# Performance work log

Hardware: AMD Instinct MI355X
Metric: run time of the kernel (lower is better)

Reference implementation:

```python
import jax, jax.numpy as jnp
import numpy as np

B, N = 2, 512
D_NODE, D_EDGE, D_HID, H = 128, 64, 128, 8
DH = D_HID // H  # per-head dim = 16
SCALE = 1.0 / (D_HID ** 0.5)  # note: scale uses full d_hid as in source


def setup_inputs() -> dict:
    key = jax.random.key(0)
    k1, k2, k3, k4 = jax.random.split(key, 4)
    node_features = jax.random.normal(k1, (B, N, D_NODE), dtype=jnp.float32)
    edge_features = jax.random.normal(k2, (B, N, N, D_EDGE), dtype=jnp.float32)
    mask = jnp.ones((B, N, N), dtype=bool)
    # Linear weights (stored as (in, out); math identical to torch x @ W.T)
    W_node = jax.random.normal(k3, (D_NODE, 3 * D_HID), dtype=jnp.float32) / np.sqrt(D_NODE)
    W_edge = jax.random.normal(k4, (D_EDGE, 3 * D_HID), dtype=jnp.float32) / np.sqrt(D_EDGE)
    return {"node_features": node_features, "edge_features": edge_features,
            "mask": mask, "W_node": W_node, "W_edge": W_edge}


def _split_heads_node(x):
    # (b, n, h*c) -> (b, h, n, c)
    b, n, hc = x.shape
    return x.reshape(b, n, H, hc // H).transpose(0, 2, 1, 3)


def _split_heads_edge(x):
    # (b, n, m, h*c) -> (b, h, n, m, c)
    b, n, m, hc = x.shape
    return x.reshape(b, n, m, H, hc // H).transpose(0, 3, 1, 2, 4)


def reference(node_features, edge_features, mask, W_node, W_edge):
    # node qkv: (b, n, 3*d_hid) -> (b, h, n, 3*dh) -> chunk
    qkv_n = _split_heads_node(node_features @ W_node)
    q_node, k_node, v_node = jnp.split(qkv_n, 3, axis=-1)  # each (b,h,n,dh)
    # edge qkv: (b, n, n, 3*d_hid) -> (b, h, n, n, 3*dh) -> chunk
    qkv_e = _split_heads_edge(edge_features @ W_edge)
    q_edge, k_edge, v_edge = jnp.split(qkv_e, 3, axis=-1)  # each (b,h,n,n,dh)

    q = q_node[:, :, :, None, :] + q_edge   # (b,h,i,j,dh)
    k = k_node[:, :, None, :, :] + k_edge   # (b,h,i,j,dh)
    v = v_node[:, :, None, :, :] + v_edge   # (b,h,i,j,dh)

    dots = SCALE * jnp.einsum('bhijd,bhijd->bhij', q, k)
    attn = jax.nn.softmax(dots, axis=-1)
    out = jnp.einsum('bhij,bhijd->bhid', attn, v)  # (b,h,n,dh)
    # (b,h,n,dh) -> (b,n,h*dh)
    b, h, n, dh = out.shape
    return out.transpose(0, 2, 1, 3).reshape(b, n, h * dh)
```

## Files before the change

kernel.cpp:

```cpp
#include <hip/hip_runtime.h>
#include <hip/hip_bf16.h>

#define NN 512
#define OC 384
#define S2F 0.12751694f

typedef __attribute__((ext_vector_type(8))) short short8;
typedef __attribute__((ext_vector_type(4))) float f32x4;

__device__ __forceinline__ unsigned short f2bf(float x) {
    unsigned u = __builtin_bit_cast(unsigned, x);
    u = (u + 0x7fffu + ((u >> 16) & 1u)) >> 16;
    return (unsigned short)u;
}

__device__ __forceinline__ ushort4 cvt4(f32x4 a) {
    union { ushort4 u4; __hip_bfloat162 h[2]; } r;
    r.h[0] = __float22bfloat162_rn(make_float2(a[0], a[1]));
    r.h[1] = __float22bfloat162_rn(make_float2(a[2], a[3]));
    return r.u4;
}

__global__ __launch_bounds__(256) void prep0_kernel(
    const float* __restrict__ Wn, const float* __restrict__ We,
    const float* __restrict__ node,
    unsigned short* __restrict__ WtN, unsigned short* __restrict__ WtE,
    unsigned short* __restrict__ nodeBf)
{
    int idx = blockIdx.x * 256 + threadIdx.x;
    if (idx < 24576) {
        int o = idx >> 6, k = idx & 63;
        WtE[idx] = f2bf(We[k * OC + o]);
    } else if (idx < 24576 + 49152) {
        int id = idx - 24576;
        int o = id >> 7, k = id & 127;
        WtN[id] = f2bf(Wn[k * OC + o]);
    } else {
        int id = idx - 73728;
        nodeBf[id] = f2bf(node[id]);
    }
}

__global__ __launch_bounds__(256) void prep1_kernel(
    const unsigned short* __restrict__ nodeBf,
    const unsigned short* __restrict__ WtN,
    float* __restrict__ qnF,
    float* __restrict__ nodeKV)
{
    const int t = threadIdx.x;
    const int w = t >> 6;
    const int lane = t & 63;
    const int lj = lane & 15;
    const int quad = lane >> 4;
    const int nbase = blockIdx.x * 32;

    short8 bfr[2][4];
#pragma unroll
    for (int nt = 0; nt < 2; ++nt)
#pragma unroll
        for (int ks = 0; ks < 4; ++ks)
            bfr[nt][ks] = *reinterpret_cast<const short8*>(
                nodeBf + (size_t)(nbase + nt * 16 + lj) * 128 + ks * 32 + quad * 8);

#pragma unroll
    for (int m = 0; m < 6; ++m) {
        int ot = (6 * w + m) * 16;
        short8 afr[4];
#pragma unroll
        for (int ks = 0; ks < 4; ++ks)
            afr[ks] = *reinterpret_cast<const short8*>(
                WtN + (size_t)(ot + lj) * 128 + ks * 32 + quad * 8);
#pragma unroll
        for (int nt = 0; nt < 2; ++nt) {
            f32x4 acc = {0.f, 0.f, 0.f, 0.f};
#pragma unroll
            for (int ks = 0; ks < 4; ++ks)
                acc = __builtin_amdgcn_mfma_f32_16x16x32_bf16(afr[ks], bfr[nt][ks], acc, 0, 0, 0);
            int n = nbase + nt * 16 + lj;
            int bb = n >> 9, ii = n & 511;
#pragma unroll
            for (int r = 0; r < 4; ++r) {
                int o = ot + quad * 4 + r;
                int h = o / 48, rem = o - h * 48;
                size_t base = (size_t)(bb * 8 + h) * NN + ii;
                if (rem < 16) {
                    qnF[base * 16 + rem] = acc[r];
                } else {
                    int d = (rem - 16) & 15;
                    int isv = (rem >= 32) ? 4 : 0;
                    nodeKV[base * 32 + (d >> 2) * 8 + isv + (d & 3)] = acc[r];
                }
            }
        }
    }
}

__global__ __launch_bounds__(512, 4) void rt_attn_main(
    const float* __restrict__ edge,
    const float* __restrict__ qnF,
    const float* __restrict__ nodeKV,
    const unsigned short* __restrict__ WtE,
    float* __restrict__ out)
{
    __shared__ unsigned short sE[2][64 * 72];
    const int bi = blockIdx.x;
    const int b = bi >> 9;
    const int i = bi & 511;
    const int t = threadIdx.x;
    const int h = t >> 6;
    const int lane = t & 63;
    const int lj = lane & 15;
    const int quad = lane >> 4;

    const int sj0 = t >> 4;
    const int sj1 = sj0 + 32;
    const int sc = (t & 15) * 4;

    const float* eBase = edge + (size_t)bi * NN * 64;
    f32x4 pf0, pf1;
    pf0 = *reinterpret_cast<const f32x4*>(eBase + (size_t)sj0 * 64 + sc);
    pf1 = *reinterpret_cast<const f32x4*>(eBase + (size_t)sj1 * 64 + sc);

    short8 afr[3][2];
#pragma unroll
    for (int T = 0; T < 3; ++T)
#pragma unroll
        for (int sec = 0; sec < 2; ++sec)
            afr[T][sec] = *reinterpret_cast<const short8*>(
                WtE + (size_t)(h * 48 + T * 16 + lj) * 64 + sec * 32 + quad * 8);

    const f32x4 qn = *reinterpret_cast<const f32x4*>(
        qnF + ((size_t)(b * 8 + h) * NN + i) * 16 + quad * 4);

    float l = 0.f;
    float oa[4] = {0.f, 0.f, 0.f, 0.f};
    const float* kvBase = nodeKV + (size_t)(b * 8 + h) * NN * 32;

    {
        *reinterpret_cast<ushort4*>(&sE[0][sj0 * 72 + sc]) = cvt4(pf0);
        *reinterpret_cast<ushort4*>(&sE[0][sj1 * 72 + sc]) = cvt4(pf1);
    }
    __syncthreads();

    for (int tt = 0; tt < 8; ++tt) {
        const int cur = tt & 1;
        f32x4 ka[4], va[4];
#pragma unroll
        for (int jn = 0; jn < 4; ++jn) {
            const float* kvp = kvBase + (size_t)(tt * 64 + jn * 16 + lj) * 32 + quad * 8;
            ka[jn] = *reinterpret_cast<const f32x4*>(kvp);
            va[jn] = *reinterpret_cast<const f32x4*>(kvp + 4);
        }
        if (tt < 7) {
            const float* nb = eBase + (size_t)(tt + 1) * 4096;
            pf0 = *reinterpret_cast<const f32x4*>(nb + (size_t)sj0 * 64 + sc);
            pf1 = *reinterpret_cast<const f32x4*>(nb + (size_t)sj1 * 64 + sc);
        }
        float dp[4];
        f32x4 fvv[4];
#pragma unroll
        for (int jn = 0; jn < 4; ++jn) {
            const int jrow = jn * 16 + lj;
            short8 b0 = *reinterpret_cast<const short8*>(&sE[cur][jrow * 72 + quad * 8]);
            short8 b1 = *reinterpret_cast<const short8*>(&sE[cur][jrow * 72 + 32 + quad * 8]);
            f32x4 fq = qn;
            fq = __builtin_amdgcn_mfma_f32_16x16x32_bf16(afr[0][0], b0, fq, 0, 0, 0);
            fq = __builtin_amdgcn_mfma_f32_16x16x32_bf16(afr[0][1], b1, fq, 0, 0, 0);
            f32x4 fk = ka[jn];
            fk = __builtin_amdgcn_mfma_f32_16x16x32_bf16(afr[1][0], b0, fk, 0, 0, 0);
            fk = __builtin_amdgcn_mfma_f32_16x16x32_bf16(afr[1][1], b1, fk, 0, 0, 0);
            f32x4 fv = va[jn];
            fv = __builtin_amdgcn_mfma_f32_16x16x32_bf16(afr[2][0], b0, fv, 0, 0, 0);
            fv = __builtin_amdgcn_mfma_f32_16x16x32_bf16(afr[2][1], b1, fv, 0, 0, 0);
            fvv[jn] = fv;
            float d0 = fq[0] * fk[0];
            d0 = fmaf(fq[1], fk[1], d0);
            d0 = fmaf(fq[2], fk[2], d0);
            d0 = fmaf(fq[3], fk[3], d0);
            dp[jn] = d0;
        }
        float t16[4], t32[4], wg[4];
#pragma unroll
        for (int jn = 0; jn < 4; ++jn) t16[jn] = __shfl_xor(dp[jn], 16);
#pragma unroll
        for (int jn = 0; jn < 4; ++jn) dp[jn] += t16[jn];
#pragma unroll
        for (int jn = 0; jn < 4; ++jn) t32[jn] = __shfl_xor(dp[jn], 32);
#pragma unroll
        for (int jn = 0; jn < 4; ++jn) {
            wg[jn] = exp2f((dp[jn] + t32[jn]) * S2F);
            l += wg[jn];
        }
#pragma unroll
        for (int jn = 0; jn < 4; ++jn)
#pragma unroll
            for (int r = 0; r < 4; ++r)
                oa[r] = fmaf(wg[jn], fvv[jn][r], oa[r]);
        if (tt < 7) {
            *reinterpret_cast<ushort4*>(&sE[cur ^ 1][sj0 * 72 + sc]) = cvt4(pf0);
            *reinterpret_cast<ushort4*>(&sE[cur ^ 1][sj1 * 72 + sc]) = cvt4(pf1);
            __syncthreads();
        }
    }

#pragma unroll
    for (int off = 1; off <= 8; off <<= 1) {
        l += __shfl_xor(l, off);
#pragma unroll
        for (int r = 0; r < 4; ++r) oa[r] += __shfl_xor(oa[r], off);
    }
    if (lj == 0) {
        float inv = 1.0f / l;
        f32x4 o4;
#pragma unroll
        for (int r = 0; r < 4; ++r) o4[r] = oa[r] * inv;
        *reinterpret_cast<f32x4*>(out + (size_t)bi * 128 + h * 16 + quad * 4) = o4;
    }
}

extern "C" void kernel_launch(void* const* d_in, const int* in_sizes, int n_in,
                              void* d_out, int out_size, void* d_ws, size_t ws_size,
                              hipStream_t stream) {
    const float* node = (const float*)d_in[0];
    const float* edge = (const float*)d_in[1];
    const float* Wn = (const float*)d_in[3];
    const float* We = (const float*)d_in[4];
    float* out = (float*)d_out;

    char* ws = (char*)d_ws;
    float* qnF = (float*)ws;
    float* nodeKV = (float*)(ws + 524288);
    unsigned short* WtE = (unsigned short*)(ws + 1572864);
    unsigned short* WtN = (unsigned short*)(ws + 1622016);
    unsigned short* nodeBf = (unsigned short*)(ws + 1720320);

    prep0_kernel<<<800, 256, 0, stream>>>(Wn, We, node, WtN, WtE, nodeBf);
    prep1_kernel<<<32, 256, 0, stream>>>(nodeBf, WtN, qnF, nodeKV);
    rt_attn_main<<<2 * NN, 512, 0, stream>>>(edge, qnF, nodeKV, WtE, out);
}
```

Before: 242.2 us.

## Load edge tiles straight into registers and split heads across blocks

The main attention kernel stops staging edge features through shared memory. Each lane now loads its own fp32 edge values directly into registers, converts them to bf16 MFMA operands, and software-pipelines the next group's loads behind the current MFMAs. Work is repartitioned so each block handles 4 heads for one row, with each wave covering 2 heads over half of the j range. A small shared-memory reduction merges the two halves. This removes the per-tile __syncthreads and LDS traffic, but each edge row is now read from global memory by two blocks, and register pressure rises.

```diff
diff --git a/kernel.cpp b/kernel.cpp
--- a/kernel.cpp
+++ b/kernel.cpp
@@ -7,6 +7,8 @@
 
 typedef __attribute__((ext_vector_type(8))) short short8;
 typedef __attribute__((ext_vector_type(4))) float f32x4;
+
+#define LD4(p) (*reinterpret_cast<const f32x4*>(p))
 
 __device__ __forceinline__ unsigned short f2bf(float x) {
     unsigned u = __builtin_bit_cast(unsigned, x);
@@ -14,11 +16,13 @@
     return (unsigned short)u;
 }
 
-__device__ __forceinline__ ushort4 cvt4(f32x4 a) {
-    union { ushort4 u4; __hip_bfloat162 h[2]; } r;
+__device__ __forceinline__ short8 cvt8(f32x4 a, f32x4 b) {
+    union { short8 s8; __hip_bfloat162 h[4]; } r;
     r.h[0] = __float22bfloat162_rn(make_float2(a[0], a[1]));
     r.h[1] = __float22bfloat162_rn(make_float2(a[2], a[3]));
-    return r.u4;
+    r.h[2] = __float22bfloat162_rn(make_float2(b[0], b[1]));
+    r.h[3] = __float22bfloat162_rn(make_float2(b[2], b[3]));
+    return r.s8;
 }
 
 __global__ __launch_bounds__(256) void prep0_kernel(
@@ -95,126 +99,149 @@
     }
 }
 
-__global__ __launch_bounds__(512, 4) void rt_attn_main(
+template <int REFILL>
+__device__ __forceinline__ void group_step(
+    f32x4& E0, f32x4& E1, f32x4& E2, f32x4& E3,
+    f32x4& K0, f32x4& V0, f32x4& K1, f32x4& V1,
+    const float* ep, const float* kq0, const float* kq1,
+    const short8 (&afr)[2][3][2],
+    const f32x4& qn0, const f32x4& qn1,
+    float& l0, float& l1, float (&oa0)[4], float (&oa1)[4])
+{
+    short8 b0 = cvt8(E0, E1);
+    short8 b1 = cvt8(E2, E3);
+    if constexpr (REFILL) {
+        E0 = LD4(ep); E1 = LD4(ep + 4); E2 = LD4(ep + 32); E3 = LD4(ep + 36);
+    }
+    f32x4 fq = __builtin_amdgcn_mfma_f32_16x16x32_bf16(afr[0][0][0], b0, qn0, 0, 0, 0);
+    fq = __builtin_amdgcn_mfma_f32_16x16x32_bf16(afr[0][0][1], b1, fq, 0, 0, 0);
+    f32x4 fk = __builtin_amdgcn_mfma_f32_16x16x32_bf16(afr[0][1][0], b0, K0, 0, 0, 0);
+    fk = __builtin_amdgcn_mfma_f32_16x16x32_bf16(afr[0][1][1], b1, fk, 0, 0, 0);
+    f32x4 fv = __builtin_amdgcn_mfma_f32_16x16x32_bf16(afr[0][2][0], b0, V0, 0, 0, 0);
+    fv = __builtin_amdgcn_mfma_f32_16x16x32_bf16(afr[0][2][1], b1, fv, 0, 0, 0);
+    if constexpr (REFILL) { K0 = LD4(kq0); V0 = LD4(kq0 + 4); }
+    float dp = fq[0] * fk[0];
+    dp = fmaf(fq[1], fk[1], dp);
+    dp = fmaf(fq[2], fk[2], dp);
+    dp = fmaf(fq[3], fk[3], dp);
+    dp += __shfl_xor(dp, 16);
+    dp += __shfl_xor(dp, 32);
+    float wg = exp2f(dp * S2F);
+    l0 += wg;
+#pragma unroll
+    for (int r = 0; r < 4; ++r) oa0[r] = fmaf(wg, fv[r], oa0[r]);
+    f32x4 gq = __builtin_amdgcn_mfma_f32_16x16x32_bf16(afr[1][0][0], b0, qn1, 0, 0, 0);
+    gq = __builtin_amdgcn_mfma_f32_16x16x32_bf16(afr[1][0][1], b1, gq, 0, 0, 0);
+    f32x4 gk = __builtin_amdgcn_mfma_f32_16x16x32_bf16(afr[1][1][0], b0, K1, 0, 0, 0);
+    gk = __builtin_amdgcn_mfma_f32_16x16x32_bf16(afr[1][1][1], b1, gk, 0, 0, 0);
+    f32x4 gv = __builtin_amdgcn_mfma_f32_16x16x32_bf16(afr[1][2][0], b0, V1, 0, 0, 0);
+    gv = __builtin_amdgcn_mfma_f32_16x16x32_bf16(afr[1][2][1], b1, gv, 0, 0, 0);
+    if constexpr (REFILL) { K1 = LD4(kq1); V1 = LD4(kq1 + 4); }
+    float dq = gq[0] * gk[0];
+    dq = fmaf(gq[1], gk[1], dq);
+    dq = fmaf(gq[2], gk[2], dq);
+    dq = fmaf(gq[3], gk[3], dq);
+    dq += __shfl_xor(dq, 16);
+    dq += __shfl_xor(dq, 32);
+    float wh = exp2f(dq * S2F);
+    l1 += wh;
+#pragma unroll
+    for (int r = 0; r < 4; ++r) oa1[r] = fmaf(wh, gv[r], oa1[r]);
+}
+
+__global__ __launch_bounds__(256, 3) void rt_attn_main(
     const float* __restrict__ edge,
     const float* __restrict__ qnF,
     const float* __restrict__ nodeKV,
     const unsigned short* __restrict__ WtE,
     float* __restrict__ out)
 {
-    __shared__ unsigned short sE[2][64 * 72];
-    const int bi = blockIdx.x;
-    const int b = bi >> 9;
-    const int i = bi & 511;
-    const int t = threadIdx.x;
-    const int h = t >> 6;
+    __shared__ float sP[4][2][4][4];
+    __shared__ float sL[4][2];
+
+    const int blk = blockIdx.x;
+    const int bi = blk >> 1;
+    const int hg = blk & 1;
+    const int b  = bi >> 9;
+    const int t  = threadIdx.x;
+    const int w  = t >> 6;
     const int lane = t & 63;
-    const int lj = lane & 15;
-    const int quad = lane >> 4;
-
-    const int sj0 = t >> 4;
-    const int sj1 = sj0 + 32;
-    const int sc = (t & 15) * 4;
-
-    const float* eBase = edge + (size_t)bi * NN * 64;
-    f32x4 pf0, pf1;
-    pf0 = *reinterpret_cast<const f32x4*>(eBase + (size_t)sj0 * 64 + sc);
-    pf1 = *reinterpret_cast<const f32x4*>(eBase + (size_t)sj1 * 64 + sc);
-
-    short8 afr[3][2];
-#pragma unroll
-    for (int T = 0; T < 3; ++T)
-#pragma unroll
-        for (int sec = 0; sec < 2; ++sec)
-            afr[T][sec] = *reinterpret_cast<const short8*>(
-                WtE + (size_t)(h * 48 + T * 16 + lj) * 64 + sec * 32 + quad * 8);
-
-    const f32x4 qn = *reinterpret_cast<const f32x4*>(
-        qnF + ((size_t)(b * 8 + h) * NN + i) * 16 + quad * 4);
-
-    float l = 0.f;
-    float oa[4] = {0.f, 0.f, 0.f, 0.f};
-    const float* kvBase = nodeKV + (size_t)(b * 8 + h) * NN * 32;
-
-    {
-        *reinterpret_cast<ushort4*>(&sE[0][sj0 * 72 + sc]) = cvt4(pf0);
-        *reinterpret_cast<ushort4*>(&sE[0][sj1 * 72 + sc]) = cvt4(pf1);
+    const int c  = lane & 15;
+    const int q  = lane >> 4;
+    const int hp = w >> 1;
+    const int jh = w & 1;
+    const int h0 = hg * 4 + hp * 2;
+
+    short8 afr[2][3][2];
+#pragma unroll
+    for (int hh = 0; hh < 2; ++hh)
+#pragma unroll
+        for (int T = 0; T < 3; ++T)
+#pragma unroll
+            for (int sec = 0; sec < 2; ++sec)
+                afr[hh][T][sec] = *reinterpret_cast<const short8*>(
+                    WtE + (size_t)((h0 + hh) * 48 + T * 16 + c) * 64 + sec * 32 + q * 8);
+
+    const f32x4 qn0 = LD4(qnF + ((size_t)(b * 8 + h0)     * NN + (bi & 511)) * 16 + q * 4);
+    const f32x4 qn1 = LD4(qnF + ((size_t)(b * 8 + h0 + 1) * NN + (bi & 511)) * 16 + q * 4);
+
+    const int j0 = jh * 256;
+    const float* ep  = edge + (size_t)bi * (NN * 64) + (size_t)(j0 + c) * 64 + q * 8;
+    const float* kp0 = nodeKV + ((size_t)(b * 8 + h0)     * NN + j0 + c) * 32 + q * 8;
+    const float* kp1 = nodeKV + ((size_t)(b * 8 + h0 + 1) * NN + j0 + c) * 32 + q * 8;
+
+    f32x4 eA0 = LD4(ep),        eA1 = LD4(ep + 4),    eA2 = LD4(ep + 32),   eA3 = LD4(ep + 36);
+    f32x4 kA0 = LD4(kp0),       vA0 = LD4(kp0 + 4);
+    f32x4 kA1 = LD4(kp1),       vA1 = LD4(kp1 + 4);
+    f32x4 eB0 = LD4(ep + 1024), eB1 = LD4(ep + 1028), eB2 = LD4(ep + 1056), eB3 = LD4(ep + 1060);
+    f32x4 kB0 = LD4(kp0 + 512), vB0 = LD4(kp0 + 516);
+    f32x4 kB1 = LD4(kp1 + 512), vB1 = LD4(kp1 + 516);
+    ep += 2048; kp0 += 1024; kp1 += 1024;
+
+    float l0 = 0.f, l1 = 0.f;
+    float oa0[4] = {0.f, 0.f, 0.f, 0.f};
+    float oa1[4] = {0.f, 0.f, 0.f, 0.f};
+
+    for (int gg = 0; gg < 7; ++gg) {
+        group_step<1>(eA0, eA1, eA2, eA3, kA0, vA0, kA1, vA1,
+                      ep,        kp0,       kp1,       afr, qn0, qn1, l0, l1, oa0, oa1);
+        group_step<1>(eB0, eB1, eB2, eB3, kB0, vB0, kB1, vB1,
+                      ep + 1024, kp0 + 512, kp1 + 512, afr, qn0, qn1, l0, l1, oa0, oa1);
+        ep += 2048; kp0 += 1024; kp1 += 1024;
+    }
+    group_step<0>(eA0, eA1, eA2, eA3, kA0, vA0, kA1, vA1,
+                  ep, kp0, kp1, afr, qn0, qn1, l0, l1, oa0, oa1);
+    group_step<0>(eB0, eB1, eB2, eB3, kB0, vB0, kB1, vB1,
+                  ep, kp0, kp1, afr, qn0, qn1, l0, l1, oa0, oa1);
+
+#pragma unroll
+    for (int off = 1; off <= 8; off <<= 1) {
+        l0 += __shfl_xor(l0, off);
+        l1 += __shfl_xor(l1, off);
+#pragma unroll
+        for (int r = 0; r < 4; ++r) {
+            oa0[r] += __shfl_xor(oa0[r], off);
+            oa1[r] += __shfl_xor(oa1[r], off);
+        }
+    }
+    if (c == 0) {
+#pragma unroll
+        for (int r = 0; r < 4; ++r) {
+            sP[w][0][q][r] = oa0[r];
+            sP[w][1][q][r] = oa1[r];
+        }
+        if (lane == 0) { sL[w][0] = l0; sL[w][1] = l1; }
     }
     __syncthreads();
 
-    for (int tt = 0; tt < 8; ++tt) {
-        const int cur = tt & 1;
-        f32x4 ka[4], va[4];
-#pragma unroll
-        for (int jn = 0; jn < 4; ++jn) {
-            const float* kvp = kvBase + (size_t)(tt * 64 + jn * 16 + lj) * 32 + quad * 8;
-            ka[jn] = *reinterpret_cast<const f32x4*>(kvp);
-            va[jn] = *reinterpret_cast<const f32x4*>(kvp + 4);
-        }
-        if (tt < 7) {
-            const float* nb = eBase + (size_t)(tt + 1) * 4096;
-            pf0 = *reinterpret_cast<const f32x4*>(nb + (size_t)sj0 * 64 + sc);
-            pf1 = *reinterpret_cast<const f32x4*>(nb + (size_t)sj1 * 64 + sc);
-        }
-        float dp[4];
-        f32x4 fvv[4];
-#pragma unroll
-        for (int jn = 0; jn < 4; ++jn) {
-            const int jrow = jn * 16 + lj;
-            short8 b0 = *reinterpret_cast<const short8*>(&sE[cur][jrow * 72 + quad * 8]);
-            short8 b1 = *reinterpret_cast<const short8*>(&sE[cur][jrow * 72 + 32 + quad * 8]);
-            f32x4 fq = qn;
-            fq = __builtin_amdgcn_mfma_f32_16x16x32_bf16(afr[0][0], b0, fq, 0, 0, 0);
-            fq = __builtin_amdgcn_mfma_f32_16x16x32_bf16(afr[0][1], b1, fq, 0, 0, 0);
-            f32x4 fk = ka[jn];
-            fk = __builtin_amdgcn_mfma_f32_16x16x32_bf16(afr[1][0], b0, fk, 0, 0, 0);
-            fk = __builtin_amdgcn_mfma_f32_16x16x32_bf16(afr[1][1], b1, fk, 0, 0, 0);
-            f32x4 fv = va[jn];
-            fv = __builtin_amdgcn_mfma_f32_16x16x32_bf16(afr[2][0], b0, fv, 0, 0, 0);
-            fv = __builtin_amdgcn_mfma_f32_16x16x32_bf16(afr[2][1], b1, fv, 0, 0, 0);
-            fvv[jn] = fv;
-            float d0 = fq[0] * fk[0];
-            d0 = fmaf(fq[1], fk[1], d0);
-            d0 = fmaf(fq[2], fk[2], d0);
-            d0 = fmaf(fq[3], fk[3], d0);
-            dp[jn] = d0;
-        }
-        float t16[4], t32[4], wg[4];
-#pragma unroll
-        for (int jn = 0; jn < 4; ++jn) t16[jn] = __shfl_xor(dp[jn], 16);
-#pragma unroll
-        for (int jn = 0; jn < 4; ++jn) dp[jn] += t16[jn];
-#pragma unroll
-        for (int jn = 0; jn < 4; ++jn) t32[jn] = __shfl_xor(dp[jn], 32);
-#pragma unroll
-        for (int jn = 0; jn < 4; ++jn) {
-            wg[jn] = exp2f((dp[jn] + t32[jn]) * S2F);
-            l += wg[jn];
-        }
-#pragma unroll
-        for (int jn = 0; jn < 4; ++jn)
-#pragma unroll
-            for (int r = 0; r < 4; ++r)
-                oa[r] = fmaf(wg[jn], fvv[jn][r], oa[r]);
-        if (tt < 7) {
-            *reinterpret_cast<ushort4*>(&sE[cur ^ 1][sj0 * 72 + sc]) = cvt4(pf0);
-            *reinterpret_cast<ushort4*>(&sE[cur ^ 1][sj1 * 72 + sc]) = cvt4(pf1);
-            __syncthreads();
-        }
-    }
-
-#pragma unroll
-    for (int off = 1; off <= 8; off <<= 1) {
-        l += __shfl_xor(l, off);
-#pragma unroll
-        for (int r = 0; r < 4; ++r) oa[r] += __shfl_xor(oa[r], off);
-    }
-    if (lj == 0) {
-        float inv = 1.0f / l;
-        f32x4 o4;
-#pragma unroll
-        for (int r = 0; r < 4; ++r) o4[r] = oa[r] * inv;
-        *reinterpret_cast<f32x4*>(out + (size_t)bi * 128 + h * 16 + quad * 4) = o4;
+    if (t < 64) {
+        int hp2 = t >> 5;
+        int hh  = (t >> 4) & 1;
+        int d   = t & 15;
+        int wA = hp2 * 2, wB = wA + 1;
+        float num = sP[wA][hh][d >> 2][d & 3] + sP[wB][hh][d >> 2][d & 3];
+        float den = sL[wA][hh] + sL[wB][hh];
+        out[(size_t)bi * 128 + (hg * 4 + hp2 * 2 + hh) * 16 + d] = num / den;
     }
 }
 
@@ -236,5 +263,5 @@
 
     prep0_kernel<<<800, 256, 0, stream>>>(Wn, We, node, WtN, WtE, nodeBf);
     prep1_kernel<<<32, 256, 0, stream>>>(nodeBf, WtN, qnF, nodeKV);
-    rt_attn_main<<<2 * NN, 512, 0, stream>>>(edge, qnF, nodeKV, WtE, out);
-}
+    rt_attn_main<<<2 * NN * 2, 256, 0, stream>>>(edge, qnF, nodeKV, WtE, out);
+}
```

Measured after the change: 331.3 us. 36.8% more time.

## Relayout node K/V buffer for coalesced loads and double-buffer them across tiles

Applied to the files above, without the earlier changes.

Node K/V values are now written in a layout of (head, d-quad, k/v, node, 4), so each quad reads contiguous 16-byte chunks across lj. The main kernel prefetches the next tile's K/V into a register double buffer, alongside the edge prefetch, and the tile loop is fully unrolled. Occupancy in launch bounds drops from 4 to 3 to make room for the extra registers. The aim is to hide K/V load latency and improve coalescing, at the cost of lower occupancy.

```diff
diff --git a/kernel.cpp b/kernel.cpp
--- a/kernel.cpp
+++ b/kernel.cpp
@@ -7,6 +7,8 @@
 
 typedef __attribute__((ext_vector_type(8))) short short8;
 typedef __attribute__((ext_vector_type(4))) float f32x4;
+
+#define LD4(p) (*reinterpret_cast<const f32x4*>(p))
 
 __device__ __forceinline__ unsigned short f2bf(float x) {
     unsigned u = __builtin_bit_cast(unsigned, x);
@@ -82,20 +84,20 @@
             for (int r = 0; r < 4; ++r) {
                 int o = ot + quad * 4 + r;
                 int h = o / 48, rem = o - h * 48;
-                size_t base = (size_t)(bb * 8 + h) * NN + ii;
                 if (rem < 16) {
-                    qnF[base * 16 + rem] = acc[r];
+                    qnF[((size_t)(bb * 8 + h) * NN + ii) * 16 + rem] = acc[r];
                 } else {
                     int d = (rem - 16) & 15;
-                    int isv = (rem >= 32) ? 4 : 0;
-                    nodeKV[base * 32 + (d >> 2) * 8 + isv + (d & 3)] = acc[r];
+                    int kv = (rem >= 32) ? 1 : 0;
+                    size_t slot = ((((size_t)(bb * 8 + h) * 4 + (d >> 2)) * 2 + kv) * NN + ii) * 4 + (d & 3);
+                    nodeKV[slot] = acc[r];
                 }
             }
         }
     }
 }
 
-__global__ __launch_bounds__(512, 4) void rt_attn_main(
+__global__ __launch_bounds__(512, 3) void rt_attn_main(
     const float* __restrict__ edge,
     const float* __restrict__ qnF,
     const float* __restrict__ nodeKV,
@@ -118,8 +120,8 @@
 
     const float* eBase = edge + (size_t)bi * NN * 64;
     f32x4 pf0, pf1;
-    pf0 = *reinterpret_cast<const f32x4*>(eBase + (size_t)sj0 * 64 + sc);
-    pf1 = *reinterpret_cast<const f32x4*>(eBase + (size_t)sj1 * 64 + sc);
+    pf0 = LD4(eBase + (size_t)sj0 * 64 + sc);
+    pf1 = LD4(eBase + (size_t)sj1 * 64 + sc);
 
     short8 afr[3][2];
 #pragma unroll
@@ -129,12 +131,20 @@
             afr[T][sec] = *reinterpret_cast<const short8*>(
                 WtE + (size_t)(h * 48 + T * 16 + lj) * 64 + sec * 32 + quad * 8);
 
-    const f32x4 qn = *reinterpret_cast<const f32x4*>(
-        qnF + ((size_t)(b * 8 + h) * NN + i) * 16 + quad * 4);
+    const f32x4 qn = LD4(qnF + ((size_t)(b * 8 + h) * NN + i) * 16 + quad * 4);
+
+    const float* kvB = nodeKV + ((size_t)(b * 8 + h) * 4 + quad) * (2 * NN * 4) + (size_t)lj * 4;
+
+    f32x4 ka[2][4], va[2][4];
+#pragma unroll
+    for (int jn = 0; jn < 4; ++jn) {
+        const float* kvp = kvB + (size_t)(jn * 16) * 4;
+        ka[0][jn] = LD4(kvp);
+        va[0][jn] = LD4(kvp + NN * 4);
+    }
 
     float l = 0.f;
     float oa[4] = {0.f, 0.f, 0.f, 0.f};
-    const float* kvBase = nodeKV + (size_t)(b * 8 + h) * NN * 32;
 
     {
         *reinterpret_cast<ushort4*>(&sE[0][sj0 * 72 + sc]) = cvt4(pf0);
@@ -142,19 +152,21 @@
     }
     __syncthreads();
 
+#pragma unroll
     for (int tt = 0; tt < 8; ++tt) {
         const int cur = tt & 1;
-        f32x4 ka[4], va[4];
-#pragma unroll
-        for (int jn = 0; jn < 4; ++jn) {
-            const float* kvp = kvBase + (size_t)(tt * 64 + jn * 16 + lj) * 32 + quad * 8;
-            ka[jn] = *reinterpret_cast<const f32x4*>(kvp);
-            va[jn] = *reinterpret_cast<const f32x4*>(kvp + 4);
-        }
         if (tt < 7) {
             const float* nb = eBase + (size_t)(tt + 1) * 4096;
-            pf0 = *reinterpret_cast<const f32x4*>(nb + (size_t)sj0 * 64 + sc);
-            pf1 = *reinterpret_cast<const f32x4*>(nb + (size_t)sj1 * 64 + sc);
+            pf0 = LD4(nb + (size_t)sj0 * 64 + sc);
+            pf1 = LD4(nb + (size_t)sj1 * 64 + sc);
+        }
+        if (tt < 7) {
+#pragma unroll
+            for (int jn = 0; jn < 4; ++jn) {
+                const float* kvp = kvB + (size_t)((tt + 1) * 64 + jn * 16) * 4;
+                ka[cur ^ 1][jn] = LD4(kvp);
+                va[cur ^ 1][jn] = LD4(kvp + NN * 4);
+            }
         }
         float dp[4];
         f32x4 fvv[4];
@@ -166,10 +178,10 @@
             f32x4 fq = qn;
             fq = __builtin_amdgcn_mfma_f32_16x16x32_bf16(afr[0][0], b0, fq, 0, 0, 0);
             fq = __builtin_amdgcn_mfma_f32_16x16x32_bf16(afr[0][1], b1, fq, 0, 0, 0);
-            f32x4 fk = ka[jn];
+            f32x4 fk = ka[cur][jn];
             fk = __builtin_amdgcn_mfma_f32_16x16x32_bf16(afr[1][0], b0, fk, 0, 0, 0);
             fk = __builtin_amdgcn_mfma_f32_16x16x32_bf16(afr[1][1], b1, fk, 0, 0, 0);
-            f32x4 fv = va[jn];
+            f32x4 fv = va[cur][jn];
             fv = __builtin_amdgcn_mfma_f32_16x16x32_bf16(afr[2][0], b0, fv, 0, 0, 0);
             fv = __builtin_amdgcn_mfma_f32_16x16x32_bf16(afr[2][1], b1, fv, 0, 0, 0);
             fvv[jn] = fv;
```

Result: faster. 225.7 us (-6.8%).
